# Kernel tuning notes

Hardware: AMD Instinct MI355X
Metric: run time of the kernel (lower is better)

## Reference

```python
import jax, jax.numpy as jnp
import numpy as np

N_RAYS = 262144
N_BINS = 64          # bin edges per ray
N_IMPORTANCE = 128   # fine samples per ray


def setup_inputs() -> dict:
    key = jax.random.key(0)
    k1, k2, k3 = jax.random.split(key, 3)
    # bins must be sorted along last axis (bin edges): cumsum of positive steps
    steps = jax.random.uniform(k1, (N_RAYS, N_BINS), dtype=jnp.float32) + 0.01
    bins = jnp.cumsum(steps, axis=-1)
    weights = jax.random.uniform(k2, (N_RAYS, N_BINS - 1), dtype=jnp.float32)
    # u plays the role of torch.rand t_vals (deterministic=False path)
    u = jax.random.uniform(k3, (N_RAYS, N_IMPORTANCE), dtype=jnp.float32)
    return {"bins": bins, "weights": weights, "u": u, "n_importance": N_IMPORTANCE}


def reference(bins, weights, u, n_importance):
    # weights: [N, M-1]; bins: [N, M]; u: [N, n_importance]
    weights = weights + 1e-5
    pdf = weights / jnp.sum(weights, axis=-1, keepdims=True)
    cdf = jnp.cumsum(pdf, axis=-1)
    cdf = jnp.concatenate([jnp.zeros_like(cdf[..., :1]), cdf], axis=-1)  # [N, M]

    # batched binary search (torch.searchsorted, right=False -> side='left')
    idx = jax.vmap(lambda c, t: jnp.searchsorted(c, t, side='left'))(
        jax.lax.stop_gradient(cdf), u)                                   # [N, I]
    lower = jnp.maximum(idx - 1, 0)
    upper = jnp.minimum(idx, cdf.shape[-1] - 1)

    cdf_lo = jnp.take_along_axis(cdf, lower, axis=-1)
    cdf_hi = jnp.take_along_axis(cdf, upper, axis=-1)
    bins_lo = jnp.take_along_axis(bins, lower, axis=-1)
    bins_hi = jnp.take_along_axis(bins, upper, axis=-1)

    denom = cdf_hi - cdf_lo
    denom = jnp.where(denom < 1e-5, jnp.ones_like(denom), denom)
    t = (u - cdf_lo) / denom
    samples = bins_lo + t * (bins_hi - bins_lo)                          # [N, I]
    return samples
```

## Files before the change

### kernel.cpp

```cpp
#include <hip/hip_runtime.h>


constexpr int NBINS = 64;
constexpr int NW = NBINS - 1;
constexpr int NIMP = 128;
constexpr int RAYS_PER_BLOCK = 4;

template <int Ctrl, int Rm>
__device__ __forceinline__ float dppterm(float x) {
    return __int_as_float(__builtin_amdgcn_update_dpp(
        0, __float_as_int(x), Ctrl, Rm, 0xF, true));
}

__device__ __forceinline__ float rdlane(float x, int lane) {
    return __int_as_float(__builtin_amdgcn_readlane(__float_as_int(x), lane));
}

__device__ __forceinline__ float wave_incl_scan(float x) {
    x += dppterm<0x111, 0xF>(x);
    x += dppterm<0x112, 0xF>(x);
    x += dppterm<0x114, 0xF>(x);
    x += dppterm<0x118, 0xF>(x);
    x += dppterm<0x142, 0xA>(x);
    x += dppterm<0x143, 0xC>(x);
    return x;
}

__global__ __launch_bounds__(256) void sample_pdf_kernel(
    const float* __restrict__ bins,
    const float* __restrict__ weights,
    const float* __restrict__ u,
    float* __restrict__ out,
    int n_rays)
{
    __shared__ float s_cdf[RAYS_PER_BLOCK][NBINS];
    __shared__ float s_bins[RAYS_PER_BLOCK][NBINS];

    const int wave = threadIdx.x >> 6;
    const int lane = threadIdx.x & 63;
    int ray = blockIdx.x * RAYS_PER_BLOCK + wave;
    if (ray >= n_rays) ray = n_rays - 1;

    const float bv = bins[(size_t)ray * NBINS + lane];
    s_bins[wave][lane] = bv;

    const float w = (lane < NW) ? (weights[(size_t)ray * NW + lane] + 1e-5f) : 0.0f;
    const float S = wave_incl_scan(w);
    const float T = rdlane(S, NW - 1);
    const float cdfv = S / T;

    if (lane < NW) s_cdf[wave][lane + 1] = cdfv;
    if (lane == NW) s_cdf[wave][0] = 0.0f;

    const float c8  = rdlane(cdfv, 7);
    const float c16 = rdlane(cdfv, 15);
    const float c24 = rdlane(cdfv, 23);
    const float c32 = rdlane(cdfv, 31);
    const float c40 = rdlane(cdfv, 39);
    const float c48 = rdlane(cdfv, 47);
    const float c56 = rdlane(cdfv, 55);

    const float* __restrict__ cdf = s_cdf[wave];
    const float* __restrict__ bn  = s_bins[wave];

    const float2 uu = ((const float2*)(u + (size_t)ray * NIMP))[lane];
    float2 res;

    #pragma unroll
    for (int k = 0; k < 2; ++k) {
        const float uv = (k == 0) ? uu.x : uu.y;

        int pos = 0;
        float lo = 0.0f;
        const bool b1 = (c32 < uv);
        if (b1) { pos = 32; lo = c32; }
        const float m2 = b1 ? c48 : c16;
        const bool b2 = (m2 < uv);
        if (b2) { pos += 16; lo = m2; }
        const float m3 = b2 ? (b1 ? c56 : c24) : (b1 ? c40 : c8);
        const bool b3 = (m3 < uv);
        if (b3) { pos += 8; lo = m3; }

        #pragma unroll
        for (int s = 4; s >= 1; s >>= 1) {
            const float val = cdf[pos + s];
            if (val < uv) { pos += s; lo = val; }
        }

        const int upper = (uv > 0.0f) ? (pos + 1) : 0;
        const float chi = cdf[upper];
        const float blo = bn[pos];
        const float bhi = bn[upper];

        float denom = chi - lo;
        denom = (denom < 1e-5f) ? 1.0f : denom;
        const float t = (uv - lo) / denom;
        const float sm = blo + t * (bhi - blo);
        if (k == 0) res.x = sm; else res.y = sm;
    }

    ((float2*)(out + (size_t)ray * NIMP))[lane] = res;
}

extern "C" void kernel_launch(void* const* d_in, const int* in_sizes, int n_in,
                              void* d_out, int out_size, void* d_ws, size_t ws_size,
                              hipStream_t stream) {
    const float* bins    = (const float*)d_in[0];
    const float* weights = (const float*)d_in[1];
    const float* u       = (const float*)d_in[2];
    float* out = (float*)d_out;

    const int n_rays = in_sizes[0] / NBINS;
    const int grid = (n_rays + RAYS_PER_BLOCK - 1) / RAYS_PER_BLOCK;
    sample_pdf_kernel<<<grid, 256, 0, stream>>>(bins, weights, u, out, n_rays);
}
```

Measured before the change: 325.5 us.

## Replace binary search with linear count plus vector LDS loads and bpermute gathers

The kernel now stores an exclusive-scan CDF, with the last lane forced to 1, in LDS. The search counts over seven register splitters and one 8-wide float4 LDS group instead of a dependent binary search. Bin and CDF values are gathered with ds_bpermute instead of a separate bins LDS array, all global loads are issued before the scan, and the divides become hardware reciprocal approximations. This shortens the dependent LDS-load chain and raises memory-level parallelism, at the cost of more compares and an approximate reciprocal that can differ slightly in precision.

```diff
diff --git a/kernel.cpp b/kernel.cpp
--- a/kernel.cpp
+++ b/kernel.cpp
@@ -14,6 +14,11 @@
 
 __device__ __forceinline__ float rdlane(float x, int lane) {
     return __int_as_float(__builtin_amdgcn_readlane(__float_as_int(x), lane));
+}
+
+__device__ __forceinline__ float bperm_f(float x, int lane_idx) {
+    return __int_as_float(
+        __builtin_amdgcn_ds_bpermute(lane_idx << 2, __float_as_int(x)));
 }
 
 __device__ __forceinline__ float wave_incl_scan(float x) {
@@ -33,73 +38,70 @@
     float* __restrict__ out,
     int n_rays)
 {
-    __shared__ float s_cdf[RAYS_PER_BLOCK][NBINS];
-    __shared__ float s_bins[RAYS_PER_BLOCK][NBINS];
+    __shared__ alignas(16) float s_cdf[RAYS_PER_BLOCK][NBINS];
 
     const int wave = threadIdx.x >> 6;
     const int lane = threadIdx.x & 63;
     int ray = blockIdx.x * RAYS_PER_BLOCK + wave;
     if (ray >= n_rays) ray = n_rays - 1;
+    const uint32_t rb = (uint32_t)ray;
 
-    const float bv = bins[(size_t)ray * NBINS + lane];
-    s_bins[wave][lane] = bv;
+    const float bv = bins[rb * NBINS + lane];
+    const float w = (lane < NW) ? (weights[rb * NW + lane] + 1e-5f) : 0.0f;
+    const float2 uu = ((const float2*)u)[rb * (NIMP / 2) + lane];
 
-    const float w = (lane < NW) ? (weights[(size_t)ray * NW + lane] + 1e-5f) : 0.0f;
     const float S = wave_incl_scan(w);
-    const float T = rdlane(S, NW - 1);
-    const float cdfv = S / T;
+    const float T = rdlane(S, 63);
+    const float rcpT = __builtin_amdgcn_rcpf(T);
+    float cdfv = (S - w) * rcpT;
+    if (lane == NBINS - 1) cdfv = 1.0f;
 
-    if (lane < NW) s_cdf[wave][lane + 1] = cdfv;
-    if (lane == NW) s_cdf[wave][0] = 0.0f;
+    s_cdf[wave][lane] = cdfv;
 
-    const float c8  = rdlane(cdfv, 7);
-    const float c16 = rdlane(cdfv, 15);
-    const float c24 = rdlane(cdfv, 23);
-    const float c32 = rdlane(cdfv, 31);
-    const float c40 = rdlane(cdfv, 39);
-    const float c48 = rdlane(cdfv, 47);
-    const float c56 = rdlane(cdfv, 55);
+    const float c8  = rdlane(cdfv, 8);
+    const float c16 = rdlane(cdfv, 16);
+    const float c24 = rdlane(cdfv, 24);
+    const float c32 = rdlane(cdfv, 32);
+    const float c40 = rdlane(cdfv, 40);
+    const float c48 = rdlane(cdfv, 48);
+    const float c56 = rdlane(cdfv, 56);
 
-    const float* __restrict__ cdf = s_cdf[wave];
-    const float* __restrict__ bn  = s_bins[wave];
-
-    const float2 uu = ((const float2*)(u + (size_t)ray * NIMP))[lane];
+    const float* cdf = s_cdf[wave];
     float2 res;
 
     #pragma unroll
     for (int k = 0; k < 2; ++k) {
         const float uv = (k == 0) ? uu.x : uu.y;
 
-        int pos = 0;
-        float lo = 0.0f;
-        const bool b1 = (c32 < uv);
-        if (b1) { pos = 32; lo = c32; }
-        const float m2 = b1 ? c48 : c16;
-        const bool b2 = (m2 < uv);
-        if (b2) { pos += 16; lo = m2; }
-        const float m3 = b2 ? (b1 ? c56 : c24) : (b1 ? c40 : c8);
-        const bool b3 = (m3 < uv);
-        if (b3) { pos += 8; lo = m3; }
+        const int grp = (int)(c8 < uv) + (int)(c16 < uv) + (int)(c24 < uv) +
+                        (int)(c32 < uv) + (int)(c40 < uv) + (int)(c48 < uv) +
+                        (int)(c56 < uv);
+        const int pos = grp << 3;
 
-        #pragma unroll
-        for (int s = 4; s >= 1; s >>= 1) {
-            const float val = cdf[pos + s];
-            if (val < uv) { pos += s; lo = val; }
-        }
+        const float4 g0 = *(const float4*)(cdf + pos);
+        const float4 g1 = *(const float4*)(cdf + pos + 4);
 
-        const int upper = (uv > 0.0f) ? (pos + 1) : 0;
-        const float chi = cdf[upper];
-        const float blo = bn[pos];
-        const float bhi = bn[upper];
+        const int cnt = (int)(g0.y < uv) + (int)(g0.z < uv) + (int)(g0.w < uv) +
+                        (int)(g1.x < uv) + (int)(g1.y < uv) + (int)(g1.z < uv) +
+                        (int)(g1.w < uv);
+
+        const int lower = pos + cnt;
+        const int upper = (uv > 0.0f) ? (lower + 1) : 0;
+
+        const float lo  = bperm_f(cdfv, lower);
+        const float chi = bperm_f(cdfv, upper);
+        const float blo = bperm_f(bv, lower);
+        const float bhi = bperm_f(bv, upper);
 
         float denom = chi - lo;
         denom = (denom < 1e-5f) ? 1.0f : denom;
-        const float t = (uv - lo) / denom;
-        const float sm = blo + t * (bhi - blo);
-        if (k == 0) res.x = sm; else res.y = sm;
+        const float t = (uv - lo) * __builtin_amdgcn_rcpf(denom);
+        const float sm = __builtin_fmaf(t, bhi - blo, blo);
+        if (k == 0) res.x = sm;
+        else        res.y = sm;
     }
 
-    ((float2*)(out + (size_t)ray * NIMP))[lane] = res;
+    ((float2*)out)[rb * (NIMP / 2) + lane] = res;
 }
 
 extern "C" void kernel_launch(void* const* d_in, const int* in_sizes, int n_in,
```

New measurement: 320.5 us. About the same (-1.5%).
